# Kernel tuning notes

Measured on AMD Instinct MI355X. Metric: run time of the kernel, lower is better.

## Reference

```python
import jax, jax.numpy as jnp
import numpy as np

L = 5        # num_layers
D = 128      # emb_dim
H = 2 * D    # mlp hidden
N_ATOM_FEATS, ATOM_VOCAB = 9, 120
N_BOND_FEATS, BOND_VOCAB = 3, 6
BN_EPS = 1e-5


def setup_inputs() -> dict:
    key = jax.random.key(0)
    ks = jax.random.split(key, 16)
    N, E = 200000, 400000
    x = jax.random.randint(ks[0], (N, N_ATOM_FEATS), 0, ATOM_VOCAB)
    edge_index = jax.random.randint(ks[1], (2, E), 0, N)
    edge_attr = jax.random.randint(ks[2], (E, N_BOND_FEATS), 0, BOND_VOCAB)
    s = 0.02
    return {
        "x": x,
        "edge_index": edge_index,
        "edge_attr": edge_attr,
        "atom_emb": jax.random.normal(ks[3], (N_ATOM_FEATS, ATOM_VOCAB, D), jnp.float32) * s,
        "bond_emb": jax.random.normal(ks[4], (L, N_BOND_FEATS, BOND_VOCAB, D), jnp.float32) * s,
        "W1": jax.random.normal(ks[5], (L, D, H), jnp.float32) * s,
        "b1": jnp.zeros((L, H), jnp.float32),
        "bn1_g": jnp.ones((L, H), jnp.float32),
        "bn1_b": jnp.zeros((L, H), jnp.float32),
        "W2": jax.random.normal(ks[6], (L, H, D), jnp.float32) * s,
        "b2": jnp.zeros((L, D), jnp.float32),
        "eps": jnp.zeros((L,), jnp.float32),
        "out_bn_g": jnp.ones((L, D), jnp.float32),
        "out_bn_b": jnp.zeros((L, D), jnp.float32),
    }


def _batchnorm(z, g, b):
    mu = jnp.mean(z, axis=0, keepdims=True)
    var = jnp.var(z, axis=0, keepdims=True)
    return (z - mu) * jax.lax.rsqrt(var + BN_EPS) * g + b


def _multi_embed(tables, idx):
    # tables: [F, V, D], idx: [N, F] -> sum_f tables[f][idx[:, f]] : [N, D]
    gathered = jax.vmap(lambda tab, i: tab[i], in_axes=(0, 1))(tables, idx)  # [F, N, D]
    return jnp.sum(gathered, axis=0)


def reference(x, edge_index, edge_attr, atom_emb, bond_emb, W1, b1, bn1_g, bn1_b,
              W2, b2, eps, out_bn_g, out_bn_b):
    N = x.shape[0]
    src, dst = edge_index[0], edge_index[1]
    h = _multi_embed(atom_emb, x)  # AtomEncoder: [N, D]
    for l in range(L):
        e = _multi_embed(bond_emb[l], edge_attr)          # BondEncoder: [E, D]
        msg = jax.nn.relu(h[src] + e)                     # message
        aggr = jax.ops.segment_sum(msg, dst, num_segments=N)  # scatter-add
        z = (1.0 + eps[l]) * h + aggr                     # GIN combine
        z = jax.nn.relu(_batchnorm(z @ W1[l] + b1[l], bn1_g[l], bn1_b[l]))
        z = z @ W2[l] + b2[l]
        h = jax.nn.relu(_batchnorm(z, out_bn_g[l], out_bn_b[l]))  # relu+dropout(p=0)
    return h  # JK='last'
```

## Files before the change

kernel.cpp:

```cpp
#include <hip/hip_runtime.h>

#define NF_ATOM 9
#define NF_BOND 3
#define DD 128
#define HH 256
#define NLAYER 5
#define NSHARD 32
#define NCODE 216

typedef float fv4 __attribute__((ext_vector_type(4)));
typedef __bf16 bfv8 __attribute__((ext_vector_type(8)));
typedef unsigned int uv4 __attribute__((ext_vector_type(4)));

__device__ inline unsigned short f2bf(float f) {
    unsigned int u = __builtin_bit_cast(unsigned int, f);
    u = u + 0x7FFFu + ((u >> 16) & 1u);
    return (unsigned short)(u >> 16);
}
__device__ inline float bf2f(unsigned short s) {
    unsigned int u = ((unsigned int)s) << 16;
    return __builtin_bit_cast(float, u);
}

__global__ __launch_bounds__(256) void k_atom(const int* __restrict__ x,
        const float* __restrict__ emb, unsigned short* __restrict__ h, int N) {
    int gid = blockIdx.x * 256 + threadIdx.x;
    int n = gid >> 5;
    if (n >= N) return;
    int c = (gid & 31) << 2;
    const int* xr = x + n * NF_ATOM;
    float4 acc = make_float4(0.f, 0.f, 0.f, 0.f);
#pragma unroll
    for (int f = 0; f < NF_ATOM; ++f) {
        int idx = xr[f];
        float4 v = *(const float4*)(emb + ((size_t)(f * 120 + idx) * DD) + c);
        acc.x += v.x; acc.y += v.y; acc.z += v.z; acc.w += v.w;
    }
    ushort4 o;
    o.x = f2bf(acc.x); o.y = f2bf(acc.y); o.z = f2bf(acc.z); o.w = f2bf(acc.w);
    *(ushort4*)(h + (size_t)n * DD + c) = o;
}

__global__ __launch_bounds__(256) void k_wconv(const float* __restrict__ W1,
        const float* __restrict__ W2, unsigned short* __restrict__ W1t,
        unsigned short* __restrict__ W2t) {
    int id = blockIdx.x * 256 + threadIdx.x;
    const int T1 = NLAYER * 4 * 256 * 32;
    if (id < T1) {
        int k = id & 31, n = (id >> 5) & 255, kc = (id >> 13) & 3, l = id >> 15;
        W1t[id] = f2bf(W1[((size_t)(l * 128 + kc * 32 + k)) * 256 + n]);
    } else {
        int id2 = id - T1;
        if (id2 >= NLAYER * 8 * 128 * 32) return;
        int k = id2 & 31, n = (id2 >> 5) & 127, kc = (id2 >> 12) & 7, l = id2 >> 15;
        W2t[id2] = f2bf(W2[((size_t)(l * 256 + kc * 32 + k)) * 128 + n]);
    }
}

__global__ __launch_bounds__(256) void k_bsumtab(const float* __restrict__ bemb,
        float* __restrict__ tab) {
    int id = blockIdx.x * 256 + threadIdx.x;
    if (id >= NLAYER * NCODE * DD) return;
    int c = id & 127;
    int code = (id >> 7) % NCODE;
    int l = id / (NCODE * DD);
    int a0 = code % 6, a1 = (code / 6) % 6, a2 = code / 36;
    const float* bl = bemb + (size_t)l * NF_BOND * 6 * DD;
    tab[id] = bl[(0 * 6 + a0) * DD + c] + bl[(1 * 6 + a1) * DD + c] + bl[(2 * 6 + a2) * DD + c];
}

__global__ __launch_bounds__(256) void k_deg(const int* __restrict__ ei, int* __restrict__ deg, int E) {
    int e = blockIdx.x * 256 + threadIdx.x;
    if (e < E) atomicAdd(&deg[ei[E + e]], 1);
}
__global__ __launch_bounds__(256) void k_bsum(const int* __restrict__ deg, int* __restrict__ bsum, int N) {
    __shared__ int red[256];
    int t = threadIdx.x, b = blockIdx.x;
    int i0 = b * 1024 + t * 4;
    int s = 0;
#pragma unroll
    for (int j = 0; j < 4; ++j) if (i0 + j < N) s += deg[i0 + j];
    red[t] = s; __syncthreads();
    for (int off = 128; off > 0; off >>= 1) {
        if (t < off) red[t] += red[t + off];
        __syncthreads();
    }
    if (t == 0) bsum[b] = red[0];
}
__global__ __launch_bounds__(256) void k_bscan(const int* __restrict__ bsum, int* __restrict__ boff, int nb) {
    __shared__ int ts[256];
    int t = threadIdx.x;
    int v = (t < nb) ? bsum[t] : 0;
    ts[t] = v; __syncthreads();
    for (int off = 1; off < 256; off <<= 1) {
        int u = (t >= off) ? ts[t - off] : 0;
        __syncthreads();
        ts[t] += u;
        __syncthreads();
    }
    if (t < nb) boff[t] = ts[t] - v;
}
__global__ __launch_bounds__(256) void k_csr(const int* deg, const int* __restrict__ boff,
        int* rs, int N, int E) {
    __shared__ int ts[256];
    int t = threadIdx.x, b = blockIdx.x;
    int i0 = b * 1024 + t * 4;
    int d[4];
#pragma unroll
    for (int j = 0; j < 4; ++j) d[j] = (i0 + j < N) ? deg[i0 + j] : 0;
    int tsum = d[0] + d[1] + d[2] + d[3];
    ts[t] = tsum; __syncthreads();
    for (int off = 1; off < 256; off <<= 1) {
        int u = (t >= off) ? ts[t - off] : 0;
        __syncthreads();
        ts[t] += u;
        __syncthreads();
    }
    int base = boff[b] + ts[t] - tsum;
    int p = 0;
#pragma unroll
    for (int j = 0; j < 4; ++j) {
        int dj = d[j];
        if (i0 + j < N) rs[i0 + j] = base + p;
        p += dj;
    }
    if (b == 0 && t == 0) rs[N] = E;
}
__global__ __launch_bounds__(256) void k_scatter(const int* __restrict__ ei,
        const int* __restrict__ ea, int* __restrict__ rs, int* __restrict__ epack, int E) {
    int e = blockIdx.x * 256 + threadIdx.x;
    if (e < E) {
        int pos = atomicAdd(&rs[ei[E + e]], 1);
        int code = ea[e * 3 + 0] + 6 * ea[e * 3 + 1] + 36 * ea[e * 3 + 2];
        epack[pos] = ei[e] | (code << 18);
    }
}

__global__ __launch_bounds__(256) void k_red(const float* __restrict__ sh,
        float* __restrict__ out, int C) {
    int t = blockIdx.x * 256 + threadIdx.x;
    if (t >= C) return;
    float a = 0.f;
#pragma unroll
    for (int s = 0; s < NSHARD; ++s) a += sh[s * C + t];
    out[t] = a;
}

__global__ __launch_bounds__(256) void k_zbuild(const unsigned short* __restrict__ y2h,
        const int* __restrict__ rs, const int* __restrict__ epack,
        const float* __restrict__ btab, const float* __restrict__ sumprev,
        const float* __restrict__ gprev, const float* __restrict__ bprev,
        const float* __restrict__ epsv, int l, int mode, float invN,
        unsigned short* __restrict__ z, int N) {
    int gid = blockIdx.x * 256 + threadIdx.x;
    int n = gid >> 5;
    if (n >= N) return;
    int c = (gid & 31) << 2;
    float sc4[4] = {1.f, 1.f, 1.f, 1.f}, sh4[4] = {0.f, 0.f, 0.f, 0.f};
    if (mode) {
#pragma unroll
        for (int j = 0; j < 4; ++j) {
            float mu = sumprev[c + j] * invN;
            float var = sumprev[DD + c + j] * invN - mu * mu;
            float r = rsqrtf(var + 1e-5f);
            float sc = gprev[c + j] * r;
            sc4[j] = sc; sh4[j] = bprev[c + j] - mu * sc;
        }
    }
    int p0 = (n == 0) ? 0 : rs[n - 1];
    int p1 = rs[n];
    float ag[4] = {0.f, 0.f, 0.f, 0.f};
    for (int p = p0; p < p1; ++p) {
        int rec = epack[p];
        int src = rec & 0x3FFFF;
        int code = ((unsigned int)rec) >> 18;
        ushort4 hv = *(const ushort4*)(y2h + (size_t)src * DD + c);
        float4 bv = *(const float4*)(btab + (size_t)code * DD + c);
        float hs[4] = {bf2f(hv.x), bf2f(hv.y), bf2f(hv.z), bf2f(hv.w)};
        if (mode) {
#pragma unroll
            for (int j = 0; j < 4; ++j) hs[j] = fmaxf(hs[j] * sc4[j] + sh4[j], 0.f);
        }
        ag[0] += fmaxf(hs[0] + bv.x, 0.f);
        ag[1] += fmaxf(hs[1] + bv.y, 0.f);
        ag[2] += fmaxf(hs[2] + bv.z, 0.f);
        ag[3] += fmaxf(hs[3] + bv.w, 0.f);
    }
    float ep = 1.0f + epsv[l];
    ushort4 sv = *(const ushort4*)(y2h + (size_t)n * DD + c);
    float hz[4] = {bf2f(sv.x), bf2f(sv.y), bf2f(sv.z), bf2f(sv.w)};
    if (mode) {
#pragma unroll
        for (int j = 0; j < 4; ++j) hz[j] = fmaxf(hz[j] * sc4[j] + sh4[j], 0.f);
    }
    ushort4 o;
    o.x = f2bf(ep * hz[0] + ag[0]);
    o.y = f2bf(ep * hz[1] + ag[1]);
    o.z = f2bf(ep * hz[2] + ag[2]);
    o.w = f2bf(ep * hz[3] + ag[3]);
    *(ushort4*)(z + (size_t)n * DD + c) = o;
}

__global__ __launch_bounds__(256) void k_gemm1(const unsigned short* __restrict__ z,
        const unsigned short* __restrict__ W1l, const float* __restrict__ bias,
        unsigned short* __restrict__ y1, float* __restrict__ shard, int N) {
    __shared__ uv4 zt[64 * 16];
    __shared__ uv4 wt[256 * 4];
    int tid = threadIdx.x;
    int row0 = blockIdx.x * 64;
    int wave = tid >> 6, lane = tid & 63, lq = lane >> 4, lr = lane & 15;
    int rbase = tid >> 4, gz = tid & 15;

    uv4 zr[4];
#pragma unroll
    for (int i = 0; i < 4; ++i)
        zr[i] = *(const uv4*)(z + (size_t)(row0 + i * 16 + rbase) * DD + gz * 8);
    const uv4* wsrc = (const uv4*)W1l;
    uv4 wr[4];
#pragma unroll
    for (int i = 0; i < 4; ++i) wr[i] = wsrc[i * 256 + tid];
#pragma unroll
    for (int i = 0; i < 4; ++i) {
        int row = i * 16 + rbase;
        zt[row * 16 + (gz ^ (row & 15))] = zr[i];
    }

    fv4 acc[4][4];
#pragma unroll
    for (int m = 0; m < 4; ++m)
#pragma unroll
        for (int nb = 0; nb < 4; ++nb) acc[m][nb] = (fv4){0.f, 0.f, 0.f, 0.f};

    for (int kc = 0; kc < 4; ++kc) {
        __syncthreads();
#pragma unroll
        for (int i = 0; i < 4; ++i) {
            int g = i * 256 + tid;
            int wn = g >> 2, gw = g & 3;
            wt[wn * 4 + (gw ^ ((wn >> 1) & 3))] = wr[i];
        }
        __syncthreads();
        if (kc < 3) {
#pragma unroll
            for (int i = 0; i < 4; ++i) wr[i] = wsrc[(size_t)(kc + 1) * 1024 + i * 256 + tid];
        }
        bfv8 a[4], b[4];
#pragma unroll
        for (int m = 0; m < 4; ++m) {
            int row = m * 16 + lr;
            a[m] = __builtin_bit_cast(bfv8, zt[row * 16 + ((kc * 4 + lq) ^ (row & 15))]);
        }
#pragma unroll
        for (int nb = 0; nb < 4; ++nb) {
            int col = wave * 64 + nb * 16 + lr;
            b[nb] = __builtin_bit_cast(bfv8, wt[col * 4 + (lq ^ ((col >> 1) & 3))]);
        }
#pragma unroll
        for (int m = 0; m < 4; ++m)
#pragma unroll
            for (int nb = 0; nb < 4; ++nb)
                acc[m][nb] = __builtin_amdgcn_mfma_f32_16x16x32_bf16(a[m], b[nb], acc[m][nb], 0, 0, 0);
    }

    float bv[4], s[4], q[4];
#pragma unroll
    for (int nb = 0; nb < 4; ++nb) {
        bv[nb] = bias[wave * 64 + nb * 16 + lr];
        s[nb] = 0.f; q[nb] = 0.f;
    }
#pragma unroll
    for (int m = 0; m < 4; ++m)
#pragma unroll
        for (int nb = 0; nb < 4; ++nb) {
            int col = wave * 64 + nb * 16 + lr;
#pragma unroll
            for (int r = 0; r < 4; ++r) {
                float v = acc[m][nb][r] + bv[nb];
                unsigned short ub = f2bf(v);
                float vr = bf2f(ub);
                int row = row0 + m * 16 + lq * 4 + r;
                y1[(size_t)row * HH + col] = ub;
                s[nb] += vr; q[nb] += vr * vr;
            }
        }
#pragma unroll
    for (int nb = 0; nb < 4; ++nb) {
        s[nb] += __shfl_xor(s[nb], 16); s[nb] += __shfl_xor(s[nb], 32);
        q[nb] += __shfl_xor(q[nb], 16); q[nb] += __shfl_xor(q[nb], 32);
    }
    if (lane < 16) {
        int shb = (blockIdx.x & (NSHARD - 1)) * 512;
#pragma unroll
        for (int nb = 0; nb < 4; ++nb) {
            int col = wave * 64 + nb * 16 + lr;
            atomicAdd(shard + shb + col, s[nb]);
            atomicAdd(shard + shb + 256 + col, q[nb]);
        }
    }
}

__global__ __launch_bounds__(256) void k_gemm2(const unsigned short* __restrict__ y1,
        const unsigned short* __restrict__ W2l, const float* __restrict__ bias,
        const float* __restrict__ sum1, const float* __restrict__ bn1g,
        const float* __restrict__ bn1b, float invN,
        unsigned short* __restrict__ y2h, float* __restrict__ shard, int N) {
    __shared__ uv4 at[64 * 32];
    __shared__ uv4 wt[128 * 4];
    int tid = threadIdx.x;
    int row0 = blockIdx.x * 64;
    int wave = tid >> 6, lane = tid & 63, lq = lane >> 4, lr = lane & 15;
    int rbase = tid >> 5, g = tid & 31;

    uv4 raw[8];
#pragma unroll
    for (int i = 0; i < 8; ++i)
        raw[i] = *((const uv4*)y1 + (size_t)(row0 + i * 8 + rbase) * 32 + g);
    const uv4* wbase = (const uv4*)W2l;
    uv4 wr[2];
    wr[0] = wbase[tid]; wr[1] = wbase[256 + tid];

    int g0 = g * 8;
    float scr[8], shr[8];
#pragma unroll
    for (int j = 0; j < 8; ++j) {
        float mu = sum1[g0 + j] * invN;
        float var = sum1[256 + g0 + j] * invN - mu * mu;
        float r = rsqrtf(var + 1e-5f);
        float sc = bn1g[g0 + j] * r;
        scr[j] = sc; shr[j] = bn1b[g0 + j] - mu * sc;
    }

#pragma unroll
    for (int i = 0; i < 8; ++i) {
        int row = i * 8 + rbase;
        uv4 p;
#pragma unroll
        for (int j = 0; j < 4; ++j) {
            float f0 = fmaxf(bf2f((unsigned short)(raw[i][j] & 0xFFFFu)) * scr[2 * j] + shr[2 * j], 0.f);
            float f1 = fmaxf(bf2f((unsigned short)(raw[i][j] >> 16)) * scr[2 * j + 1] + shr[2 * j + 1], 0.f);
            p[j] = (unsigned int)f2bf(f0) | ((unsigned int)f2bf(f1) << 16);
        }
        at[row * 32 + (g ^ (row & 15))] = p;
    }

    fv4 acc[4][2];
#pragma unroll
    for (int m = 0; m < 4; ++m) { acc[m][0] = (fv4){0.f,0.f,0.f,0.f}; acc[m][1] = (fv4){0.f,0.f,0.f,0.f}; }

    for (int kc = 0; kc < 8; ++kc) {
        __syncthreads();
        {
            int g2 = tid, wn = g2 >> 2, gw = g2 & 3;
            wt[wn * 4 + (gw ^ ((wn >> 1) & 3))] = wr[0];
            int g3 = 256 + tid, wn3 = g3 >> 2, gw3 = g3 & 3;
            wt[wn3 * 4 + (gw3 ^ ((wn3 >> 1) & 3))] = wr[1];
        }
        __syncthreads();
        if (kc < 7) {
            wr[0] = wbase[(size_t)(kc + 1) * 512 + tid];
            wr[1] = wbase[(size_t)(kc + 1) * 512 + 256 + tid];
        }
        bfv8 a[4], b[2];
#pragma unroll
        for (int m = 0; m < 4; ++m) {
            int row = m * 16 + lr;
            a[m] = __builtin_bit_cast(bfv8, at[row * 32 + ((kc * 4 + lq) ^ (row & 15))]);
        }
#pragma unroll
        for (int nb = 0; nb < 2; ++nb) {
            int col = wave * 32 + nb * 16 + lr;
            b[nb] = __builtin_bit_cast(bfv8, wt[col * 4 + (lq ^ ((col >> 1) & 3))]);
        }
#pragma unroll
        for (int m = 0; m < 4; ++m)
#pragma unroll
            for (int nb = 0; nb < 2; ++nb)
                acc[m][nb] = __builtin_amdgcn_mfma_f32_16x16x32_bf16(a[m], b[nb], acc[m][nb], 0, 0, 0);
    }

    float bv[2], s[2], q[2];
#pragma unroll
    for (int nb = 0; nb < 2; ++nb) {
        bv[nb] = bias[wave * 32 + nb * 16 + lr];
        s[nb] = 0.f; q[nb] = 0.f;
    }
#pragma unroll
    for (int m = 0; m < 4; ++m)
#pragma unroll
        for (int nb = 0; nb < 2; ++nb) {
            int col = wave * 32 + nb * 16 + lr;
#pragma unroll
            for (int r = 0; r < 4; ++r) {
                float v = acc[m][nb][r] + bv[nb];
                unsigned short ub = f2bf(v);
                float vr = bf2f(ub);
                int row = row0 + m * 16 + lq * 4 + r;
                y2h[(size_t)row * DD + col] = ub;
                s[nb] += vr; q[nb] += vr * vr;
            }
        }
#pragma unroll
    for (int nb = 0; nb < 2; ++nb) {
        s[nb] += __shfl_xor(s[nb], 16); s[nb] += __shfl_xor(s[nb], 32);
        q[nb] += __shfl_xor(q[nb], 16); q[nb] += __shfl_xor(q[nb], 32);
    }
    if (lane < 16) {
        int shb = (blockIdx.x & (NSHARD - 1)) * 256;
#pragma unroll
        for (int nb = 0; nb < 2; ++nb) {
            int col = wave * 32 + nb * 16 + lr;
            atomicAdd(shard + shb + col, s[nb]);
            atomicAdd(shard + shb + 128 + col, q[nb]);
        }
    }
}

__global__ __launch_bounds__(256) void k_bnfinal(const unsigned short* __restrict__ y2h,
        const float* __restrict__ sum2, const float* __restrict__ g,
        const float* __restrict__ b, float* __restrict__ out, float invN, int N) {
    __shared__ float scS[128], shS[128];
    int tid = threadIdx.x;
    if (tid < 128) {
        float mu = sum2[tid] * invN;
        float var = sum2[128 + tid] * invN - mu * mu;
        float r = rsqrtf(var + 1e-5f);
        float sc = g[tid] * r;
        scS[tid] = sc; shS[tid] = b[tid] - mu * sc;
    }
    __syncthreads();
    size_t base = ((size_t)blockIdx.x * 256 + tid) * 4;
    if (base >= (size_t)N * DD) return;
    int c = (int)(base & (DD - 1));
    ushort4 v = *(const ushort4*)(y2h + base);
    float4 o;
    o.x = fmaxf(bf2f(v.x) * scS[c] + shS[c], 0.f);
    o.y = fmaxf(bf2f(v.y) * scS[c + 1] + shS[c + 1], 0.f);
    o.z = fmaxf(bf2f(v.z) * scS[c + 2] + shS[c + 2], 0.f);
    o.w = fmaxf(bf2f(v.w) * scS[c + 3] + shS[c + 3], 0.f);
    *(float4*)(out + base) = o;
}

extern "C" void kernel_launch(void* const* d_in, const int* in_sizes, int n_in,
                              void* d_out, int out_size, void* d_ws, size_t ws_size,
                              hipStream_t stream) {
    const int* x = (const int*)d_in[0];
    const int* ei = (const int*)d_in[1];
    const int* ea = (const int*)d_in[2];
    const float* atom_emb = (const float*)d_in[3];
    const float* bond_emb = (const float*)d_in[4];
    const float* W1 = (const float*)d_in[5];
    const float* b1 = (const float*)d_in[6];
    const float* bn1_g = (const float*)d_in[7];
    const float* bn1_b = (const float*)d_in[8];
    const float* W2 = (const float*)d_in[9];
    const float* b2 = (const float*)d_in[10];
    const float* epsv = (const float*)d_in[11];
    const float* obn_g = (const float*)d_in[12];
    const float* obn_b = (const float*)d_in[13];
    int N = in_sizes[0] / NF_ATOM;
    int E = in_sizes[1] / 2;

    char* wsb = (char*)d_ws;
    unsigned short* y2h = (unsigned short*)wsb;
    unsigned short* zb = (unsigned short*)(wsb + (size_t)N * 256);
    unsigned short* y1b = (unsigned short*)(wsb + (size_t)N * 512);
    int* epack = (int*)(wsb + (size_t)N * 1024);
    unsigned short* w1t = (unsigned short*)(wsb + (size_t)N * 1024 + (size_t)E * 4);
    unsigned short* w2t = w1t + 163840;
    int* rsarr = (int*)(w2t + 163840);
    int* bsum = rsarr + (N + 1);
    int* boff = bsum + 256;
    float* st = (float*)(boff + 256);
    float* shard1 = st + NLAYER * 768;
    float* shard2 = shard1 + NSHARD * 512;
    float* btab = shard2 + NSHARD * 256;
    float invN = 1.0f / (float)N;
    int nbk = (N + 1023) / 1024;

    k_wconv<<<1280, 256, 0, stream>>>(W1, W2, w1t, w2t);
    k_bsumtab<<<(NLAYER * NCODE * DD + 255) / 256, 256, 0, stream>>>(bond_emb, btab);
    hipMemsetAsync(rsarr, 0, ((size_t)N + 1) * 4, stream);
    k_deg<<<(E + 255) / 256, 256, 0, stream>>>(ei, rsarr, E);
    k_bsum<<<nbk, 256, 0, stream>>>(rsarr, bsum, N);
    k_bscan<<<1, 256, 0, stream>>>(bsum, boff, nbk);
    k_csr<<<nbk, 256, 0, stream>>>(rsarr, boff, rsarr, N, E);
    k_scatter<<<(E + 255) / 256, 256, 0, stream>>>(ei, ea, rsarr, epack, E);
    k_atom<<<(N * 32 + 255) / 256, 256, 0, stream>>>(x, atom_emb, y2h, N);

    int gb = N / 64;
    for (int l = 0; l < NLAYER; ++l) {
        float* sum1 = st + l * 768;
        float* sum2 = st + l * 768 + 512;
        const float* sumprev = (l == 0) ? st : (st + (l - 1) * 768 + 512);
        const float* gprev = (l == 0) ? obn_g : (obn_g + (l - 1) * DD);
        const float* bprev = (l == 0) ? obn_b : (obn_b + (l - 1) * DD);
        hipMemsetAsync(shard1, 0, (size_t)NSHARD * 768 * sizeof(float), stream);
        k_zbuild<<<(N * 32 + 255) / 256, 256, 0, stream>>>(y2h, rsarr, epack,
                btab + (size_t)l * NCODE * DD, sumprev, gprev, bprev,
                epsv, l, (l == 0) ? 0 : 1, invN, zb, N);
        k_gemm1<<<gb, 256, 0, stream>>>(zb, w1t + (size_t)l * 32768,
                b1 + l * HH, y1b, shard1, N);
        k_red<<<2, 256, 0, stream>>>(shard1, sum1, 512);
        k_gemm2<<<gb, 256, 0, stream>>>(y1b, w2t + (size_t)l * 32768, b2 + l * DD,
                sum1, bn1_g + l * HH, bn1_b + l * HH, invN, y2h, shard2, N);
        k_red<<<1, 256, 0, stream>>>(shard2, sum2, 256);
    }
    k_bnfinal<<<(int)(((size_t)N * DD / 4 + 255) / 256), 256, 0, stream>>>(
            y2h, st + 4 * 768 + 512, obn_g + 4 * DD, obn_b + 4 * DD, (float*)d_out, invN, N);
}
```

Before: 852.2 us.

## Recompute GEMM1 inside fused MLP kernel instead of storing y1 intermediate

The first MLP GEMM now runs twice per layer. A stats-only pass gathers the BatchNorm sums without writing the N×256 hidden activations, and a fused kernel recomputes GEMM1, applies BN+ReLU in registers, stages the result through shared memory and runs GEMM2. This removes the bf16 y1 write and its read-back, at the cost of redoing GEMM1's MFMA work. BN scale and shift are now precomputed once in the reduction kernel instead of in every thread, and the edge gather loop is unrolled by two. BN1 statistics now use fp32 values rather than bf16-rounded ones, which slightly changes numerics.

```diff
diff --git a/kernel.cpp b/kernel.cpp
--- a/kernel.cpp
+++ b/kernel.cpp
@@ -136,62 +136,78 @@
     }
 }
 
-__global__ __launch_bounds__(256) void k_red(const float* __restrict__ sh,
-        float* __restrict__ out, int C) {
-    int t = blockIdx.x * 256 + threadIdx.x;
+__global__ void k_red(const float* __restrict__ sh, int C, const float* __restrict__ bng,
+        const float* __restrict__ bnb, const float* __restrict__ gbias, int useb,
+        float invN, float* __restrict__ sc_out, float* __restrict__ sh_out) {
+    int t = threadIdx.x;
     if (t >= C) return;
-    float a = 0.f;
-#pragma unroll
-    for (int s = 0; s < NSHARD; ++s) a += sh[s * C + t];
-    out[t] = a;
+    float a = 0.f, qq = 0.f;
+#pragma unroll
+    for (int s = 0; s < NSHARD; ++s) {
+        a += sh[s * 2 * C + t];
+        qq += sh[s * 2 * C + C + t];
+    }
+    float mu = a * invN;
+    float var = qq * invN - mu * mu;
+    float r = rsqrtf(var + 1e-5f);
+    float sc = bng[t] * r;
+    float shift = bnb[t] - mu * sc;
+    if (useb) shift += gbias[t] * sc;
+    sc_out[t] = sc; sh_out[t] = shift;
+}
+
+__device__ inline void edge_acc(ushort4 hv, float4 bv, float4 sc, float4 sh, int mode, float* ag) {
+    float h0 = bf2f(hv.x), h1 = bf2f(hv.y), h2 = bf2f(hv.z), h3 = bf2f(hv.w);
+    if (mode) {
+        h0 = fmaxf(h0 * sc.x + sh.x, 0.f); h1 = fmaxf(h1 * sc.y + sh.y, 0.f);
+        h2 = fmaxf(h2 * sc.z + sh.z, 0.f); h3 = fmaxf(h3 * sc.w + sh.w, 0.f);
+    }
+    ag[0] += fmaxf(h0 + bv.x, 0.f); ag[1] += fmaxf(h1 + bv.y, 0.f);
+    ag[2] += fmaxf(h2 + bv.z, 0.f); ag[3] += fmaxf(h3 + bv.w, 0.f);
 }
 
 __global__ __launch_bounds__(256) void k_zbuild(const unsigned short* __restrict__ y2h,
         const int* __restrict__ rs, const int* __restrict__ epack,
-        const float* __restrict__ btab, const float* __restrict__ sumprev,
-        const float* __restrict__ gprev, const float* __restrict__ bprev,
-        const float* __restrict__ epsv, int l, int mode, float invN,
-        unsigned short* __restrict__ z, int N) {
+        const float* __restrict__ btab, const float* __restrict__ sctab,
+        const float* __restrict__ shtab, const float* __restrict__ epsv,
+        int l, int mode, unsigned short* __restrict__ z, int N) {
     int gid = blockIdx.x * 256 + threadIdx.x;
     int n = gid >> 5;
     if (n >= N) return;
     int c = (gid & 31) << 2;
-    float sc4[4] = {1.f, 1.f, 1.f, 1.f}, sh4[4] = {0.f, 0.f, 0.f, 0.f};
-    if (mode) {
-#pragma unroll
-        for (int j = 0; j < 4; ++j) {
-            float mu = sumprev[c + j] * invN;
-            float var = sumprev[DD + c + j] * invN - mu * mu;
-            float r = rsqrtf(var + 1e-5f);
-            float sc = gprev[c + j] * r;
-            sc4[j] = sc; sh4[j] = bprev[c + j] - mu * sc;
-        }
-    }
+    float4 sc4 = make_float4(1.f, 1.f, 1.f, 1.f), sh4 = make_float4(0.f, 0.f, 0.f, 0.f);
+    if (mode) { sc4 = *(const float4*)(sctab + c); sh4 = *(const float4*)(shtab + c); }
     int p0 = (n == 0) ? 0 : rs[n - 1];
     int p1 = rs[n];
     float ag[4] = {0.f, 0.f, 0.f, 0.f};
-    for (int p = p0; p < p1; ++p) {
+    int p = p0;
+    for (; p + 2 <= p1; p += 2) {
+        int rec0 = epack[p], rec1 = epack[p + 1];
+        int s0 = rec0 & 0x3FFFF, s1 = rec1 & 0x3FFFF;
+        int c0 = ((unsigned int)rec0) >> 18, c1 = ((unsigned int)rec1) >> 18;
+        ushort4 h0 = *(const ushort4*)(y2h + (size_t)s0 * DD + c);
+        ushort4 h1 = *(const ushort4*)(y2h + (size_t)s1 * DD + c);
+        float4 b0 = *(const float4*)(btab + (size_t)c0 * DD + c);
+        float4 b1 = *(const float4*)(btab + (size_t)c1 * DD + c);
+        edge_acc(h0, b0, sc4, sh4, mode, ag);
+        edge_acc(h1, b1, sc4, sh4, mode, ag);
+    }
+    if (p < p1) {
         int rec = epack[p];
-        int src = rec & 0x3FFFF;
-        int code = ((unsigned int)rec) >> 18;
-        ushort4 hv = *(const ushort4*)(y2h + (size_t)src * DD + c);
-        float4 bv = *(const float4*)(btab + (size_t)code * DD + c);
-        float hs[4] = {bf2f(hv.x), bf2f(hv.y), bf2f(hv.z), bf2f(hv.w)};
-        if (mode) {
-#pragma unroll
-            for (int j = 0; j < 4; ++j) hs[j] = fmaxf(hs[j] * sc4[j] + sh4[j], 0.f);
-        }
-        ag[0] += fmaxf(hs[0] + bv.x, 0.f);
-        ag[1] += fmaxf(hs[1] + bv.y, 0.f);
-        ag[2] += fmaxf(hs[2] + bv.z, 0.f);
-        ag[3] += fmaxf(hs[3] + bv.w, 0.f);
+        int s0 = rec & 0x3FFFF;
+        int c0 = ((unsigned int)rec) >> 18;
+        ushort4 h0 = *(const ushort4*)(y2h + (size_t)s0 * DD + c);
+        float4 b0 = *(const float4*)(btab + (size_t)c0 * DD + c);
+        edge_acc(h0, b0, sc4, sh4, mode, ag);
     }
     float ep = 1.0f + epsv[l];
     ushort4 sv = *(const ushort4*)(y2h + (size_t)n * DD + c);
     float hz[4] = {bf2f(sv.x), bf2f(sv.y), bf2f(sv.z), bf2f(sv.w)};
     if (mode) {
-#pragma unroll
-        for (int j = 0; j < 4; ++j) hz[j] = fmaxf(hz[j] * sc4[j] + sh4[j], 0.f);
+        hz[0] = fmaxf(hz[0] * sc4.x + sh4.x, 0.f);
+        hz[1] = fmaxf(hz[1] * sc4.y + sh4.y, 0.f);
+        hz[2] = fmaxf(hz[2] * sc4.z + sh4.z, 0.f);
+        hz[3] = fmaxf(hz[3] * sc4.w + sh4.w, 0.f);
     }
     ushort4 o;
     o.x = f2bf(ep * hz[0] + ag[0]);
@@ -201,9 +217,9 @@
     *(ushort4*)(z + (size_t)n * DD + c) = o;
 }
 
-__global__ __launch_bounds__(256) void k_gemm1(const unsigned short* __restrict__ z,
+__global__ __launch_bounds__(256) void k_stat1(const unsigned short* __restrict__ z,
         const unsigned short* __restrict__ W1l, const float* __restrict__ bias,
-        unsigned short* __restrict__ y1, float* __restrict__ shard, int N) {
+        float* __restrict__ shard, int N) {
     __shared__ uv4 zt[64 * 16];
     __shared__ uv4 wt[256 * 4];
     int tid = threadIdx.x;
@@ -271,18 +287,12 @@
 #pragma unroll
     for (int m = 0; m < 4; ++m)
 #pragma unroll
-        for (int nb = 0; nb < 4; ++nb) {
-            int col = wave * 64 + nb * 16 + lr;
+        for (int nb = 0; nb < 4; ++nb)
 #pragma unroll
             for (int r = 0; r < 4; ++r) {
                 float v = acc[m][nb][r] + bv[nb];
-                unsigned short ub = f2bf(v);
-                float vr = bf2f(ub);
-                int row = row0 + m * 16 + lq * 4 + r;
-                y1[(size_t)row * HH + col] = ub;
-                s[nb] += vr; q[nb] += vr * vr;
+                s[nb] += v; q[nb] += v * v;
             }
-        }
 #pragma unroll
     for (int nb = 0; nb < 4; ++nb) {
         s[nb] += __shfl_xor(s[nb], 16); s[nb] += __shfl_xor(s[nb], 32);
@@ -299,66 +309,114 @@
     }
 }
 
-__global__ __launch_bounds__(256) void k_gemm2(const unsigned short* __restrict__ y1,
-        const unsigned short* __restrict__ W2l, const float* __restrict__ bias,
-        const float* __restrict__ sum1, const float* __restrict__ bn1g,
-        const float* __restrict__ bn1b, float invN,
+__global__ __launch_bounds__(256) void k_fgemm(const unsigned short* __restrict__ z,
+        const unsigned short* __restrict__ W1l, const unsigned short* __restrict__ W2l,
+        const float* __restrict__ sc1, const float* __restrict__ sh1,
+        const float* __restrict__ bias2,
         unsigned short* __restrict__ y2h, float* __restrict__ shard, int N) {
-    __shared__ uv4 at[64 * 32];
-    __shared__ uv4 wt[128 * 4];
+    __shared__ uv4 smem[2560];
+    uv4* zt = smem;
+    uv4* wt = smem + 1024;
+    uv4* at = smem;
+    uv4* wt2 = smem + 2048;
     int tid = threadIdx.x;
     int row0 = blockIdx.x * 64;
     int wave = tid >> 6, lane = tid & 63, lq = lane >> 4, lr = lane & 15;
-    int rbase = tid >> 5, g = tid & 31;
-
-    uv4 raw[8];
-#pragma unroll
-    for (int i = 0; i < 8; ++i)
-        raw[i] = *((const uv4*)y1 + (size_t)(row0 + i * 8 + rbase) * 32 + g);
-    const uv4* wbase = (const uv4*)W2l;
-    uv4 wr[2];
-    wr[0] = wbase[tid]; wr[1] = wbase[256 + tid];
-
-    int g0 = g * 8;
-    float scr[8], shr[8];
-#pragma unroll
-    for (int j = 0; j < 8; ++j) {
-        float mu = sum1[g0 + j] * invN;
-        float var = sum1[256 + g0 + j] * invN - mu * mu;
-        float r = rsqrtf(var + 1e-5f);
-        float sc = bn1g[g0 + j] * r;
-        scr[j] = sc; shr[j] = bn1b[g0 + j] - mu * sc;
-    }
-
-#pragma unroll
-    for (int i = 0; i < 8; ++i) {
-        int row = i * 8 + rbase;
-        uv4 p;
-#pragma unroll
-        for (int j = 0; j < 4; ++j) {
-            float f0 = fmaxf(bf2f((unsigned short)(raw[i][j] & 0xFFFFu)) * scr[2 * j] + shr[2 * j], 0.f);
-            float f1 = fmaxf(bf2f((unsigned short)(raw[i][j] >> 16)) * scr[2 * j + 1] + shr[2 * j + 1], 0.f);
-            p[j] = (unsigned int)f2bf(f0) | ((unsigned int)f2bf(f1) << 16);
-        }
-        at[row * 32 + (g ^ (row & 15))] = p;
-    }
-
-    fv4 acc[4][2];
-#pragma unroll
-    for (int m = 0; m < 4; ++m) { acc[m][0] = (fv4){0.f,0.f,0.f,0.f}; acc[m][1] = (fv4){0.f,0.f,0.f,0.f}; }
+    int rbase = tid >> 4, gz = tid & 15;
+
+    uv4 zr[4];
+#pragma unroll
+    for (int i = 0; i < 4; ++i)
+        zr[i] = *(const uv4*)(z + (size_t)(row0 + i * 16 + rbase) * DD + gz * 8);
+    const uv4* w1src = (const uv4*)W1l;
+    uv4 wr[4];
+#pragma unroll
+    for (int i = 0; i < 4; ++i) wr[i] = w1src[i * 256 + tid];
+#pragma unroll
+    for (int i = 0; i < 4; ++i) {
+        int row = i * 16 + rbase;
+        zt[row * 16 + (gz ^ (row & 15))] = zr[i];
+    }
+
+    fv4 acc1[4][4];
+#pragma unroll
+    for (int mc = 0; mc < 4; ++mc)
+#pragma unroll
+        for (int nr = 0; nr < 4; ++nr) acc1[mc][nr] = (fv4){0.f, 0.f, 0.f, 0.f};
+
+    for (int kc = 0; kc < 4; ++kc) {
+        __syncthreads();
+#pragma unroll
+        for (int i = 0; i < 4; ++i) {
+            int g = i * 256 + tid;
+            int wn = g >> 2, gw = g & 3;
+            wt[wn * 4 + (gw ^ ((wn >> 1) & 3))] = wr[i];
+        }
+        __syncthreads();
+        if (kc < 3) {
+#pragma unroll
+            for (int i = 0; i < 4; ++i) wr[i] = w1src[(size_t)(kc + 1) * 1024 + i * 256 + tid];
+        }
+        bfv8 wf[4], zf[4];
+#pragma unroll
+        for (int mc = 0; mc < 4; ++mc) {
+            int col = wave * 64 + mc * 16 + lr;
+            wf[mc] = __builtin_bit_cast(bfv8, wt[col * 4 + (lq ^ ((col >> 1) & 3))]);
+        }
+#pragma unroll
+        for (int nr = 0; nr < 4; ++nr) {
+            int row = nr * 16 + lr;
+            zf[nr] = __builtin_bit_cast(bfv8, zt[row * 16 + ((kc * 4 + lq) ^ (row & 15))]);
+        }
+#pragma unroll
+        for (int mc = 0; mc < 4; ++mc)
+#pragma unroll
+            for (int nr = 0; nr < 4; ++nr)
+                acc1[mc][nr] = __builtin_amdgcn_mfma_f32_16x16x32_bf16(wf[mc], zf[nr], acc1[mc][nr], 0, 0, 0);
+    }
+    __syncthreads();
+
+    const uv4* w2src = (const uv4*)W2l;
+    uv4 wr2[2];
+    wr2[0] = w2src[tid]; wr2[1] = w2src[256 + tid];
+
+#pragma unroll
+    for (int mc = 0; mc < 4; ++mc) {
+        int ycol0 = wave * 64 + mc * 16 + lq * 4;
+        float4 s4 = *(const float4*)(sc1 + ycol0);
+        float4 h4 = *(const float4*)(sh1 + ycol0);
+        int gg = wave * 8 + mc * 2 + (lq >> 1);
+#pragma unroll
+        for (int nr = 0; nr < 4; ++nr) {
+            int zrow = nr * 16 + lr;
+            float v0 = fmaxf(acc1[mc][nr][0] * s4.x + h4.x, 0.f);
+            float v1 = fmaxf(acc1[mc][nr][1] * s4.y + h4.y, 0.f);
+            float v2 = fmaxf(acc1[mc][nr][2] * s4.z + h4.z, 0.f);
+            float v3 = fmaxf(acc1[mc][nr][3] * s4.w + h4.w, 0.f);
+            uint2 pk;
+            pk.x = (unsigned int)f2bf(v0) | ((unsigned int)f2bf(v1) << 16);
+            pk.y = (unsigned int)f2bf(v2) | ((unsigned int)f2bf(v3) << 16);
+            int gs = gg ^ (zrow & 15);
+            ((uint2*)at)[(zrow * 32 + gs) * 2 + (lq & 1)] = pk;
+        }
+    }
+
+    fv4 acc2[4][2];
+#pragma unroll
+    for (int m = 0; m < 4; ++m) { acc2[m][0] = (fv4){0.f,0.f,0.f,0.f}; acc2[m][1] = (fv4){0.f,0.f,0.f,0.f}; }
 
     for (int kc = 0; kc < 8; ++kc) {
         __syncthreads();
         {
-            int g2 = tid, wn = g2 >> 2, gw = g2 & 3;
-            wt[wn * 4 + (gw ^ ((wn >> 1) & 3))] = wr[0];
+            int wn = tid >> 2, gw = tid & 3;
+            wt2[wn * 4 + (gw ^ ((wn >> 1) & 3))] = wr2[0];
             int g3 = 256 + tid, wn3 = g3 >> 2, gw3 = g3 & 3;
-            wt[wn3 * 4 + (gw3 ^ ((wn3 >> 1) & 3))] = wr[1];
+            wt2[wn3 * 4 + (gw3 ^ ((wn3 >> 1) & 3))] = wr2[1];
         }
         __syncthreads();
         if (kc < 7) {
-            wr[0] = wbase[(size_t)(kc + 1) * 512 + tid];
-            wr[1] = wbase[(size_t)(kc + 1) * 512 + 256 + tid];
+            wr2[0] = w2src[(size_t)(kc + 1) * 512 + tid];
+            wr2[1] = w2src[(size_t)(kc + 1) * 512 + 256 + tid];
         }
         bfv8 a[4], b[2];
 #pragma unroll
@@ -369,19 +427,19 @@
 #pragma unroll
         for (int nb = 0; nb < 2; ++nb) {
             int col = wave * 32 + nb * 16 + lr;
-            b[nb] = __builtin_bit_cast(bfv8, wt[col * 4 + (lq ^ ((col >> 1) & 3))]);
+            b[nb] = __builtin_bit_cast(bfv8, wt2[col * 4 + (lq ^ ((col >> 1) & 3))]);
         }
 #pragma unroll
         for (int m = 0; m < 4; ++m)
 #pragma unroll
             for (int nb = 0; nb < 2; ++nb)
-                acc[m][nb] = __builtin_amdgcn_mfma_f32_16x16x32_bf16(a[m], b[nb], acc[m][nb], 0, 0, 0);
+                acc2[m][nb] = __builtin_amdgcn_mfma_f32_16x16x32_bf16(a[m], b[nb], acc2[m][nb], 0, 0, 0);
     }
 
     float bv[2], s[2], q[2];
 #pragma unroll
     for (int nb = 0; nb < 2; ++nb) {
-        bv[nb] = bias[wave * 32 + nb * 16 + lr];
+        bv[nb] = bias2[wave * 32 + nb * 16 + lr];
         s[nb] = 0.f; q[nb] = 0.f;
     }
 #pragma unroll
@@ -391,7 +449,7 @@
             int col = wave * 32 + nb * 16 + lr;
 #pragma unroll
             for (int r = 0; r < 4; ++r) {
-                float v = acc[m][nb][r] + bv[nb];
+                float v = acc2[m][nb][r] + bv[nb];
                 unsigned short ub = f2bf(v);
                 float vr = bf2f(ub);
                 int row = row0 + m * 16 + lq * 4 + r;
@@ -416,27 +474,19 @@
 }
 
 __global__ __launch_bounds__(256) void k_bnfinal(const unsigned short* __restrict__ y2h,
-        const float* __restrict__ sum2, const float* __restrict__ g,
-        const float* __restrict__ b, float* __restrict__ out, float invN, int N) {
-    __shared__ float scS[128], shS[128];
-    int tid = threadIdx.x;
-    if (tid < 128) {
-        float mu = sum2[tid] * invN;
-        float var = sum2[128 + tid] * invN - mu * mu;
-        float r = rsqrtf(var + 1e-5f);
-        float sc = g[tid] * r;
-        scS[tid] = sc; shS[tid] = b[tid] - mu * sc;
-    }
-    __syncthreads();
-    size_t base = ((size_t)blockIdx.x * 256 + tid) * 4;
+        const float* __restrict__ sc2, const float* __restrict__ sh2,
+        float* __restrict__ out, int N) {
+    size_t base = ((size_t)blockIdx.x * 256 + threadIdx.x) * 4;
     if (base >= (size_t)N * DD) return;
     int c = (int)(base & (DD - 1));
     ushort4 v = *(const ushort4*)(y2h + base);
+    float4 s = *(const float4*)(sc2 + c);
+    float4 t = *(const float4*)(sh2 + c);
     float4 o;
-    o.x = fmaxf(bf2f(v.x) * scS[c] + shS[c], 0.f);
-    o.y = fmaxf(bf2f(v.y) * scS[c + 1] + shS[c + 1], 0.f);
-    o.z = fmaxf(bf2f(v.z) * scS[c + 2] + shS[c + 2], 0.f);
-    o.w = fmaxf(bf2f(v.w) * scS[c + 3] + shS[c + 3], 0.f);
+    o.x = fmaxf(bf2f(v.x) * s.x + t.x, 0.f);
+    o.y = fmaxf(bf2f(v.y) * s.y + t.y, 0.f);
+    o.z = fmaxf(bf2f(v.z) * s.z + t.z, 0.f);
+    o.w = fmaxf(bf2f(v.w) * s.w + t.w, 0.f);
     *(float4*)(out + base) = o;
 }
 
@@ -463,17 +513,19 @@
     char* wsb = (char*)d_ws;
     unsigned short* y2h = (unsigned short*)wsb;
     unsigned short* zb = (unsigned short*)(wsb + (size_t)N * 256);
-    unsigned short* y1b = (unsigned short*)(wsb + (size_t)N * 512);
-    int* epack = (int*)(wsb + (size_t)N * 1024);
-    unsigned short* w1t = (unsigned short*)(wsb + (size_t)N * 1024 + (size_t)E * 4);
+    int* epack = (int*)(wsb + (size_t)N * 512);
+    unsigned short* w1t = (unsigned short*)(wsb + (size_t)N * 512 + (size_t)E * 4);
     unsigned short* w2t = w1t + 163840;
-    int* rsarr = (int*)(w2t + 163840);
+    float* btab = (float*)((char*)w2t + 327680);
+    float* sc1 = btab + NLAYER * NCODE * DD;
+    float* sh1 = sc1 + 256;
+    float* sc2 = sh1 + 256;
+    float* sh2 = sc2 + 128;
+    float* shard1 = sh2 + 128;
+    float* shard2 = shard1 + NSHARD * 512;
+    int* rsarr = (int*)(shard2 + NSHARD * 256);
     int* bsum = rsarr + (N + 1);
     int* boff = bsum + 256;
-    float* st = (float*)(boff + 256);
-    float* shard1 = st + NLAYER * 768;
-    float* shard2 = shard1 + NSHARD * 512;
-    float* btab = shard2 + NSHARD * 256;
     float invN = 1.0f / (float)N;
     int nbk = (N + 1023) / 1024;
 
@@ -489,22 +541,17 @@
 
     int gb = N / 64;
     for (int l = 0; l < NLAYER; ++l) {
-        float* sum1 = st + l * 768;
-        float* sum2 = st + l * 768 + 512;
-        const float* sumprev = (l == 0) ? st : (st + (l - 1) * 768 + 512);
-        const float* gprev = (l == 0) ? obn_g : (obn_g + (l - 1) * DD);
-        const float* bprev = (l == 0) ? obn_b : (obn_b + (l - 1) * DD);
         hipMemsetAsync(shard1, 0, (size_t)NSHARD * 768 * sizeof(float), stream);
         k_zbuild<<<(N * 32 + 255) / 256, 256, 0, stream>>>(y2h, rsarr, epack,
-                btab + (size_t)l * NCODE * DD, sumprev, gprev, bprev,
-                epsv, l, (l == 0) ? 0 : 1, invN, zb, N);
-        k_gemm1<<<gb, 256, 0, stream>>>(zb, w1t + (size_t)l * 32768,
-                b1 + l * HH, y1b, shard1, N);
-        k_red<<<2, 256, 0, stream>>>(shard1, sum1, 512);
-        k_gemm2<<<gb, 256, 0, stream>>>(y1b, w2t + (size_t)l * 32768, b2 + l * DD,
-                sum1, bn1_g + l * HH, bn1_b + l * HH, invN, y2h, shard2, N);
-        k_red<<<1, 256, 0, stream>>>(shard2, sum2, 256);
+                btab + (size_t)l * NCODE * DD, sc2, sh2, epsv, l, (l == 0) ? 0 : 1, zb, N);
+        k_stat1<<<gb, 256, 0, stream>>>(zb, w1t + (size_t)l * 32768, b1 + l * HH, shard1, N);
+        k_red<<<1, 256, 0, stream>>>(shard1, 256, bn1_g + l * HH, bn1_b + l * HH,
+                b1 + l * HH, 1, invN, sc1, sh1);
+        k_fgemm<<<gb, 256, 0, stream>>>(zb, w1t + (size_t)l * 32768, w2t + (size_t)l * 32768,
+                sc1, sh1, b2 + l * DD, y2h, shard2, N);
+        k_red<<<1, 128, 0, stream>>>(shard2, 128, obn_g + l * DD, obn_b + l * DD,
+                (const float*)nullptr, 0, invN, sc2, sh2);
     }
     k_bnfinal<<<(int)(((size_t)N * DD / 4 + 255) / 256), 256, 0, stream>>>(
-            y2h, st + 4 * 768 + 512, obn_g + 4 * DD, obn_b + 4 * DD, (float*)d_out, invN, N);
-}
+            y2h, sc2, sh2, (float*)d_out, N);
+}
```

Result: faster. 791.3 us (-7.1%).
